# Kernel optimization log

Measured on AMD Instinct MI355X. Metric: run time of the kernel, lower is better.

## Reference

```python
import jax, jax.numpy as jnp
import numpy as np


def setup_inputs() -> dict:
    key = jax.random.key(0)
    k1, k2 = jax.random.split(key)
    S_src, S_tgt, B, H = 2048, 2048, 16, 256
    out_e = jax.random.normal(k1, (S_src, B, 2 * H), dtype=jnp.float32)
    out_d = jax.random.normal(k2, (S_tgt, B, H), dtype=jnp.float32)
    return {"out_e": out_e, "out_d": out_d}


def reference(out_e, out_d):
    # out_e: [S_src, B, 2*H] (bidirectional), out_d: [S_tgt, B, H]
    S, B, H2 = out_e.shape
    # sum the two directions: [S, B, H]
    enc = out_e.reshape(S, B, 2, H2 // 2).sum(axis=2)
    enc = enc.transpose(1, 0, 2)   # [B, S_src, H]
    dec = out_d.transpose(1, 0, 2)  # [B, S_tgt, H]
    # attn scores [B, S_src, S_tgt]; softmax over source positions (dim=1)
    attn = jnp.einsum('bsh,bth->bst', enc, dec)
    attn = jax.nn.softmax(attn, axis=1)
    # context: weighted sum over source positions -> [B, S_tgt, H]
    context = jnp.einsum('bst,bsh->bth', attn, enc)
    return context.transpose(1, 0, 2)  # [S_tgt, B, H]
```

## Files before the change

### kernel.cpp

```cpp
#include <hip/hip_runtime.h>
#include <stdint.h>
#include <stddef.h>

#define BATCH 16
#define SEQ 2048
#define HDIM 256
#define SCHUNK 32
#define TTILE 128
#define NCHUNK 64
#define TILE_U16 8192
#define NTILES 1024
#define PREBLK 2048
#define KSTRIDE 260

typedef float f32x4 __attribute__((ext_vector_type(4)));
typedef float f32x16 __attribute__((ext_vector_type(16)));
typedef _Float16 f16x8 __attribute__((ext_vector_type(8)));
typedef __bf16 bf16x8 __attribute__((ext_vector_type(8)));
typedef unsigned short u16;
typedef u16 u16x8 __attribute__((ext_vector_type(8)));
typedef unsigned int u32;
typedef u32 u32x4 __attribute__((ext_vector_type(4)));
typedef const __attribute__((address_space(1))) u32* gp1_t;
typedef __attribute__((address_space(3))) u32* lp3_t;

static __device__ __forceinline__ u16 f2bf(float f) {
  union { float f; unsigned int u; } v; v.f = f;
  unsigned int u = v.u;
  unsigned int r = u + 0x7FFFu + ((u >> 16) & 1u);
  return (u16)(r >> 16);
}

__global__ __launch_bounds__(256, 4)
void prepass_kernel(const float* __restrict__ e,
                    u16* __restrict__ KH, u16* __restrict__ VT) {
  __shared__ float Ks[16 * KSTRIDE];
  const int tid = threadIdx.x;
  const int bid = blockIdx.x;
  const int h2  = bid & 1;
  const int tb  = bid >> 1;
  const int b   = tb >> 6;
  const int ck  = tb & 63;
  const size_t tile = (size_t)tb * TILE_U16;
  const int r0 = h2 * 16;

  {
    int row = tid >> 4;
    int c16 = tid & 15;
    const float* src = e + ((size_t)(ck * SCHUNK + r0 + row) * BATCH + b) * (2 * HDIM);
#pragma unroll
    for (int u = 0; u < 4; ++u) {
      int col = c16 * 4 + 64 * u;
      float4 xa = *(const float4*)(src + col);
      float4 xb = *(const float4*)(src + col + HDIM);
      float4 s; s.x = xa.x + xb.x; s.y = xa.y + xb.y; s.z = xa.z + xb.z; s.w = xa.w + xb.w;
      *(float4*)&Ks[row * KSTRIDE + col] = s;
    }
  }
  __syncthreads();

  const int lane = tid & 63;
  const int w = tid >> 6;

  {
    int half = lane >> 5;
    int l5   = lane & 31;
    int lm   = l5 & 15;
    int g    = (l5 >> 4) & 1;
#pragma unroll
    for (int i = 0; i < 2; ++i) {
      int kb = w * 4 + i * 2 + half;
      const float* rp = &Ks[lm * KSTRIDE + kb * 16 + g * 8];
      u16x8 hi;
#pragma unroll
      for (int j = 0; j < 8; ++j)
        hi[j] = __builtin_bit_cast(u16, (_Float16)rp[j]);
      int lane_out = g * 32 + r0 + lm;
      *(u16x8*)&KH[tile + (size_t)(kb * 64 + lane_out) * 8] = hi;
    }
  }

  {
    int m = lane & 31;
    int g = lane >> 5;
#pragma unroll
    for (int i = 0; i < 2; ++i) {
      int ht = w * 2 + i;
      int fr = ht * 2 + h2;
      u16x8 v;
#pragma unroll
      for (int j = 0; j < 8; ++j)
        v[j] = f2bf(Ks[(g * 8 + j) * KSTRIDE + ht * 32 + m]);
      *(u16x8*)&VT[tile + (size_t)(fr * 64 + lane) * 8] = v;
    }
  }
}

__global__ __launch_bounds__(512, 2)
void attn_main_kernel(const u16* __restrict__ KH, const u16* __restrict__ VT,
                      const float* __restrict__ dq,
                      float* __restrict__ out) {
  __shared__ alignas(16) u16 KHs[4][TILE_U16];
  __shared__ alignas(16) u16 VTs[6][TILE_U16];

  const int tid  = threadIdx.x;
  const int lane = tid & 63;
  const int wv   = tid >> 6;
  const int wq   = wv & 3;
  const int grp  = wv >> 2;
  const int m    = lane & 31;
  const int g    = lane >> 5;

  const int bid = blockIdx.x;
  const int b  = ((bid & 7) << 1) | ((bid >> 3) & 1);
  const int t0 = (bid >> 4) * TTILE;

  const int tq = t0 + wq * 32 + m;
  const float* qp = dq + ((size_t)tq * BATCH + b) * HDIM;
  f16x8 qh[16];
#pragma unroll
  for (int kb = 0; kb < 16; ++kb) {
    int h = kb * 16 + g * 8;
    float4 f0 = *(const float4*)(qp + h);
    float4 f1 = *(const float4*)(qp + h + 4);
    float xs[8] = {f0.x, f0.y, f0.z, f0.w, f1.x, f1.y, f1.z, f1.w};
    u16x8 hb;
#pragma unroll
    for (int j = 0; j < 8; ++j)
      hb[j] = __builtin_bit_cast(u16, (_Float16)xs[j]);
    qh[kb] = __builtin_bit_cast(f16x8, hb);
  }

  f32x16 ctx[8];
#pragma unroll
  for (int ht = 0; ht < 8; ++ht) ctx[ht] = (f32x16)(0.0f);
  float dsum = 0.0f;
  bf16x8 pa0 = {}, pa1 = {};

  const bool isVT  = (wv >> 1) & 1;
  const int  choff = wv >> 2;
  const int  subbase = (wv & 1) * 8;
  const u16* srcArr = isVT ? VT : KH;
  auto stage = [&](int p) {
    int ckk = 2 * p + choff;
    int ktile = 2 * (p & 1) + choff;
    int vtile = (p % 3) * 2 + choff;
    size_t tb = ((size_t)b * NCHUNK + ckk) * TILE_U16;
    u16* dst = isVT ? &VTs[vtile][0] : &KHs[ktile][0];
#pragma unroll
    for (int i = 0; i < 8; ++i) {
      int sub = subbase + i;
      __builtin_amdgcn_global_load_lds(
          (gp1_t)(const void*)&srcArr[tb + (size_t)sub * 512 + lane * 8],
          (lp3_t)(void*)&dst[sub * 512], 16, 0, 0);
    }
  };

  auto qk = [&](int p, f32x16& a0, f32x16& a1) {
    int kt = 2 * (p & 1) + grp;
#pragma unroll
    for (int kb = 0; kb < 16; kb += 2) {
      f16x8 k0 = __builtin_bit_cast(f16x8, *(const u16x8*)&KHs[kt][kb * 512 + lane * 8]);
      f16x8 k1 = __builtin_bit_cast(f16x8, *(const u16x8*)&KHs[kt][(kb + 1) * 512 + lane * 8]);
      a0 = __builtin_amdgcn_mfma_f32_32x32x16_f16(k0, qh[kb], a0, 0, 0, 0);
      a1 = __builtin_amdgcn_mfma_f32_32x32x16_f16(k1, qh[kb + 1], a1, 0, 0, 0);
    }
  };

  auto pv = [&](int p) {
    int vt_ = (p % 3) * 2 + grp;
#pragma unroll
    for (int ht = 0; ht < 8; ++ht) {
      bf16x8 v0 = __builtin_bit_cast(bf16x8, *(const u16x8*)&VTs[vt_][(ht * 2) * 512 + lane * 8]);
      bf16x8 v1 = __builtin_bit_cast(bf16x8, *(const u16x8*)&VTs[vt_][(ht * 2 + 1) * 512 + lane * 8]);
      ctx[ht] = __builtin_amdgcn_mfma_f32_32x32x16_bf16(pa0, v0, ctx[ht], 0, 0, 0);
      ctx[ht] = __builtin_amdgcn_mfma_f32_32x32x16_bf16(pa1, v1, ctx[ht], 0, 0, 0);
    }
  };

  auto softmax_pack = [&](const f32x16& a0, const f32x16& a1) {
    float pf[16];
#pragma unroll
    for (int r = 0; r < 16; ++r) {
      pf[r] = __expf(a0[r] + a1[r] - 128.0f);
      dsum += pf[r];
    }
    u32 c[8];
#pragma unroll
    for (int q = 0; q < 8; ++q)
      asm("v_cvt_pk_bf16_f32 %0, %1, %2"
          : "=v"(c[q]) : "v"(pf[2 * q]), "v"(pf[2 * q + 1]));
    asm("v_permlane32_swap_b32 %0, %1" : "+v"(c[0]), "+v"(c[2]));
    asm("v_permlane32_swap_b32 %0, %1" : "+v"(c[1]), "+v"(c[3]));
    asm("v_permlane32_swap_b32 %0, %1" : "+v"(c[4]), "+v"(c[6]));
    asm("v_permlane32_swap_b32 %0, %1" : "+v"(c[5]), "+v"(c[7]));
    u32x4 w0 = {c[0], c[1], c[2], c[3]};
    u32x4 w1 = {c[4], c[5], c[6], c[7]};
    pa0 = __builtin_bit_cast(bf16x8, w0);
    pa1 = __builtin_bit_cast(bf16x8, w1);
  };

  stage(0);
  stage(1);
  asm volatile("s_waitcnt vmcnt(8)" ::: "memory");
  __builtin_amdgcn_s_barrier();
  {
    f32x16 a0 = (f32x16)(0.0f), a1 = (f32x16)(0.0f);
    qk(0, a0, a1);
    softmax_pack(a0, a1);
  }

  for (int j = 0; j < 32; ++j) {
    asm volatile("s_waitcnt vmcnt(0)" ::: "memory");
    __builtin_amdgcn_s_barrier();
    if (j < 30) stage(j + 2);

    f32x16 a0 = (f32x16)(0.0f), a1 = (f32x16)(0.0f);
    __builtin_amdgcn_s_setprio(1);
    if (j < 31) qk(j + 1, a0, a1);
    pv(j);
    __builtin_amdgcn_s_setprio(0);
    if (j < 31) softmax_pack(a0, a1);
  }

  dsum += __shfl_xor(dsum, 32, 64);
  __syncthreads();

  float* exch = (wq == 0) ? (float*)&KHs[0][0]
              : (wq == 1) ? (float*)&KHs[2][0]
              : (wq == 2) ? (float*)&VTs[0][0]
                          : (float*)&VTs[2][0];
  float* dex = (float*)&VTs[4][0];

  if (grp == 1) {
#pragma unroll
    for (int r4 = 0; r4 < 4; ++r4)
#pragma unroll
      for (int ht = 0; ht < 8; ++ht) {
        f32x4 v = {ctx[ht][r4 * 4], ctx[ht][r4 * 4 + 1],
                   ctx[ht][r4 * 4 + 2], ctx[ht][r4 * 4 + 3]};
        *(f32x4*)&exch[r4 * 2048 + ht * 256 + lane * 4] = v;
      }
    dex[wq * 64 + lane] = dsum;
  }
  __syncthreads();

  if (grp == 0) {
    float dB = dex[wq * 64 + lane];
    float inv = 1.0f / (dsum + dB);
#pragma unroll
    for (int r4 = 0; r4 < 4; ++r4)
#pragma unroll
      for (int ht = 0; ht < 8; ++ht) {
        f32x4 v = *(const f32x4*)&exch[r4 * 2048 + ht * 256 + lane * 4];
        ctx[ht][r4 * 4]     += v[0];
        ctx[ht][r4 * 4 + 1] += v[1];
        ctx[ht][r4 * 4 + 2] += v[2];
        ctx[ht][r4 * 4 + 3] += v[3];
      }
#pragma unroll
    for (int r = 0; r < 16; ++r) {
      int tl = (r & 3) + 8 * (r >> 2) + 4 * g;
      float rinv = __shfl(inv, tl, 64);
      int t = t0 + wq * 32 + tl;
      float* op = out + ((size_t)t * BATCH + b) * HDIM + m;
#pragma unroll
      for (int ht = 0; ht < 8; ++ht)
        op[ht * 32] = ctx[ht][r] * rinv;
    }
  }
}

extern "C" void kernel_launch(void* const* d_in, const int* in_sizes, int n_in,
                              void* d_out, int out_size, void* d_ws, size_t ws_size,
                              hipStream_t stream) {
  const float* e  = (const float*)d_in[0];
  const float* dq = (const float*)d_in[1];
  float* out = (float*)d_out;
  u16* KH = (u16*)d_ws;
  u16* VT = KH + (size_t)NTILES * TILE_U16;
  prepass_kernel<<<dim3(PREBLK), dim3(256), 0, stream>>>(e, KH, VT);
  attn_main_kernel<<<dim3(BATCH * (SEQ / TTILE)), dim3(512), 0, stream>>>(
      KH, VT, dq, out);
}
```

Before: 201.5 us.

## Fuse encoder prepass into attention kernel with a grid-wide atomic barrier

Removes the separate prepass launch. Each of the 256 attention blocks now converts four 32-row encoder chunks into the fp16 K and bf16 V^T tiles in workspace, then waits on a global atomic counter barrier before running the attention main loop. This saves a kernel launch and the gap between the two kernels. In exchange it relies on all 256 blocks being co-resident (512 threads, 2 blocks per CU), and the prepass now runs with less parallelism per block than the old 2048-block launch.

New measurement: 299.7 us. +48.7%, slower.

```diff
diff --git a/kernel.cpp b/kernel.cpp
--- a/kernel.cpp
+++ b/kernel.cpp
@@ -10,7 +10,6 @@
 #define NCHUNK 64
 #define TILE_U16 8192
 #define NTILES 1024
-#define PREBLK 2048
 #define KSTRIDE 260
 
 typedef float f32x4 __attribute__((ext_vector_type(4)));
@@ -24,6 +23,8 @@
 typedef const __attribute__((address_space(1))) u32* gp1_t;
 typedef __attribute__((address_space(3))) u32* lp3_t;
 
+__device__ unsigned int g_bar = 0;
+
 static __device__ __forceinline__ u16 f2bf(float f) {
   union { float f; unsigned int u; } v; v.f = f;
   unsigned int u = v.u;
@@ -31,75 +32,11 @@
   return (u16)(r >> 16);
 }
 
-__global__ __launch_bounds__(256, 4)
-void prepass_kernel(const float* __restrict__ e,
-                    u16* __restrict__ KH, u16* __restrict__ VT) {
-  __shared__ float Ks[16 * KSTRIDE];
-  const int tid = threadIdx.x;
-  const int bid = blockIdx.x;
-  const int h2  = bid & 1;
-  const int tb  = bid >> 1;
-  const int b   = tb >> 6;
-  const int ck  = tb & 63;
-  const size_t tile = (size_t)tb * TILE_U16;
-  const int r0 = h2 * 16;
-
-  {
-    int row = tid >> 4;
-    int c16 = tid & 15;
-    const float* src = e + ((size_t)(ck * SCHUNK + r0 + row) * BATCH + b) * (2 * HDIM);
-#pragma unroll
-    for (int u = 0; u < 4; ++u) {
-      int col = c16 * 4 + 64 * u;
-      float4 xa = *(const float4*)(src + col);
-      float4 xb = *(const float4*)(src + col + HDIM);
-      float4 s; s.x = xa.x + xb.x; s.y = xa.y + xb.y; s.z = xa.z + xb.z; s.w = xa.w + xb.w;
-      *(float4*)&Ks[row * KSTRIDE + col] = s;
-    }
-  }
-  __syncthreads();
-
-  const int lane = tid & 63;
-  const int w = tid >> 6;
-
-  {
-    int half = lane >> 5;
-    int l5   = lane & 31;
-    int lm   = l5 & 15;
-    int g    = (l5 >> 4) & 1;
-#pragma unroll
-    for (int i = 0; i < 2; ++i) {
-      int kb = w * 4 + i * 2 + half;
-      const float* rp = &Ks[lm * KSTRIDE + kb * 16 + g * 8];
-      u16x8 hi;
-#pragma unroll
-      for (int j = 0; j < 8; ++j)
-        hi[j] = __builtin_bit_cast(u16, (_Float16)rp[j]);
-      int lane_out = g * 32 + r0 + lm;
-      *(u16x8*)&KH[tile + (size_t)(kb * 64 + lane_out) * 8] = hi;
-    }
-  }
-
-  {
-    int m = lane & 31;
-    int g = lane >> 5;
-#pragma unroll
-    for (int i = 0; i < 2; ++i) {
-      int ht = w * 2 + i;
-      int fr = ht * 2 + h2;
-      u16x8 v;
-#pragma unroll
-      for (int j = 0; j < 8; ++j)
-        v[j] = f2bf(Ks[(g * 8 + j) * KSTRIDE + ht * 32 + m]);
-      *(u16x8*)&VT[tile + (size_t)(fr * 64 + lane) * 8] = v;
-    }
-  }
-}
-
 __global__ __launch_bounds__(512, 2)
-void attn_main_kernel(const u16* __restrict__ KH, const u16* __restrict__ VT,
-                      const float* __restrict__ dq,
-                      float* __restrict__ out) {
+void attn_fused_kernel(const float* __restrict__ e,
+                       u16* __restrict__ KH, u16* __restrict__ VT,
+                       const float* __restrict__ dq,
+                       float* __restrict__ out) {
   __shared__ alignas(16) u16 KHs[4][TILE_U16];
   __shared__ alignas(16) u16 VTs[6][TILE_U16];
 
@@ -111,9 +48,68 @@
   const int m    = lane & 31;
   const int g    = lane >> 5;
 
-  const int bid = blockIdx.x;
-  const int b  = ((bid & 7) << 1) | ((bid >> 3) & 1);
-  const int t0 = (bid >> 4) * TTILE;
+  const int bid  = blockIdx.x;
+  const int b    = ((bid & 7) << 1) | ((bid >> 3) & 1);
+  const int tq16 = bid >> 4;
+  const int t0   = tq16 * TTILE;
+
+  {
+    float* Ks = (float*)&KHs[0][0];
+    for (int cc = 0; cc < 4; ++cc) {
+      const int ck = tq16 * 4 + cc;
+      const size_t tile = ((size_t)b * NCHUNK + ck) * TILE_U16;
+
+      {
+        int row = tid >> 4;
+        int c16 = tid & 15;
+        const float* src = e + ((size_t)(ck * SCHUNK + row) * BATCH + b) * (2 * HDIM);
+#pragma unroll
+        for (int u = 0; u < 4; ++u) {
+          int col = c16 * 4 + 64 * u;
+          float4 xa = *(const float4*)(src + col);
+          float4 xb = *(const float4*)(src + col + HDIM);
+          float4 s; s.x = xa.x + xb.x; s.y = xa.y + xb.y;
+          s.z = xa.z + xb.z; s.w = xa.w + xb.w;
+          *(float4*)&Ks[row * KSTRIDE + col] = s;
+        }
+      }
+      __syncthreads();
+
+#pragma unroll
+      for (int i = 0; i < 2; ++i) {
+        int kb = wv * 2 + i;
+        const float* rp = &Ks[m * KSTRIDE + kb * 16 + g * 8];
+        u16x8 hi;
+#pragma unroll
+        for (int j = 0; j < 8; ++j)
+          hi[j] = __builtin_bit_cast(u16, (_Float16)rp[j]);
+        *(u16x8*)&KH[tile + (size_t)(kb * 64 + lane) * 8] = hi;
+      }
+#pragma unroll
+      for (int i = 0; i < 2; ++i) {
+        int fr = wv * 2 + i;
+        int ht = fr >> 1, ka = fr & 1;
+        u16x8 v;
+#pragma unroll
+        for (int j = 0; j < 8; ++j)
+          v[j] = f2bf(Ks[(ka * 16 + g * 8 + j) * KSTRIDE + ht * 32 + m]);
+        *(u16x8*)&VT[tile + (size_t)(fr * 64 + lane) * 8] = v;
+      }
+      __syncthreads();
+    }
+  }
+
+  __threadfence();
+  __syncthreads();
+  if (tid == 0) {
+    unsigned int old = __hip_atomic_fetch_add(&g_bar, 1u, __ATOMIC_ACQ_REL,
+                                              __HIP_MEMORY_SCOPE_AGENT);
+    unsigned int target = ((old >> 8) + 1u) << 8;
+    while (__hip_atomic_load(&g_bar, __ATOMIC_ACQUIRE,
+                             __HIP_MEMORY_SCOPE_AGENT) < target)
+      __builtin_amdgcn_s_sleep(8);
+  }
+  __syncthreads();
 
   const int tq = t0 + wq * 32 + m;
   const float* qp = dq + ((size_t)tq * BATCH + b) * HDIM;
@@ -279,7 +275,6 @@
   float* out = (float*)d_out;
   u16* KH = (u16*)d_ws;
   u16* VT = KH + (size_t)NTILES * TILE_U16;
-  prepass_kernel<<<dim3(PREBLK), dim3(256), 0, stream>>>(e, KH, VT);
-  attn_main_kernel<<<dim3(BATCH * (SEQ / TTILE)), dim3(512), 0, stream>>>(
-      KH, VT, dq, out);
+  attn_fused_kernel<<<dim3(BATCH * (SEQ / TTILE)), dim3(512), 0, stream>>>(
+      e, KH, VT, dq, out);
 }
```
